# Kernel tuning notes

Measured on AMD Instinct MI355X. Metric: run time of the kernel, lower is better.

## Reference

```python
import jax, jax.numpy as jnp
import numpy as np

N_NODES = 100000
N_EDGES = 1600000
LN_EPS = 1e-5
CLAMP = 1.8


def setup_inputs() -> dict:
    key = jax.random.key(0)
    ks = jax.random.split(key, 12)
    feats = [100, 64, 64, 47]
    inp = {
        "x": jax.random.normal(ks[0], (N_NODES, feats[0]), dtype=jnp.float32),
        "adj_vals": jax.random.uniform(ks[1], (N_EDGES,), dtype=jnp.float32),
        "adj_row": jax.random.randint(ks[2], (N_EDGES,), 0, N_NODES),
        "adj_col": jax.random.randint(ks[3], (N_EDGES,), 0, N_NODES),
        "ln_gamma": jnp.ones((feats[0],), dtype=jnp.float32),
        "ln_beta": jnp.zeros((feats[0],), dtype=jnp.float32),
    }
    for i in range(3):
        fi, fo = feats[i], feats[i + 1]
        bound = 1.0 / np.sqrt(fi)
        inp[f"W{i+1}"] = jax.random.uniform(ks[4 + 2 * i], (fi, fo), minval=-bound, maxval=bound, dtype=jnp.float32)
        inp[f"b{i+1}"] = jax.random.uniform(ks[5 + 2 * i], (fo,), minval=-bound, maxval=bound, dtype=jnp.float32)
    return inp


def _spmm(vals, row, col, x):
    # out[i] = sum_{e: row[e]==i} vals[e] * x[col[e]]
    gathered = vals[:, None] * x[col]  # [E, D]
    return jax.ops.segment_sum(gathered, row, num_segments=N_NODES)


def reference(x, adj_vals, adj_row, adj_col, ln_gamma, ln_beta, W1, b1, W2, b2, W3, b3):
    # clamp to [-1.8, 1.8]: relu(x+1.8)-1.8 then 1.8-relu(1.8-x)
    x = jnp.clip(x, -CLAMP, CLAMP)
    # LayerNorm over last dim (100)
    mu = jnp.mean(x, axis=-1, keepdims=True)
    var = jnp.mean(jnp.square(x - mu), axis=-1, keepdims=True)
    x = (x - mu) * jax.lax.rsqrt(var + LN_EPS) * ln_gamma + ln_beta
    # GCN layers: Linear -> spmm -> (elu except last); dropout=0 => identity
    x = jax.nn.elu(_spmm(adj_vals, adj_row, adj_col, x @ W1 + b1))
    x = jax.nn.elu(_spmm(adj_vals, adj_row, adj_col, x @ W2 + b2))
    x = _spmm(adj_vals, adj_row, adj_col, x @ W3 + b3)
    return x
```

## Files before the change

kernel.cpp:

```cpp
#include <hip/hip_runtime.h>
#include <cstdint>
#include <cstddef>

#define N_NODES_C 100000
#define N_EDGES_C 1600000
#define LN_EPS_C 1e-5f
#define CLAMP_C 1.8f
#define SC_BLOCKS 1024
#define LN_BLOCKS 1024

typedef unsigned short ushort_t;

__device__ __forceinline__ float readlane_f(float v, int l) {
  return __uint_as_float(__builtin_amdgcn_readlane(__float_as_uint(v), l));
}

__device__ __forceinline__ float wave_sum(float v) {
#pragma unroll
  for (int off = 32; off > 0; off >>= 1) v += __shfl_xor(v, off, 64);
  return v;
}

__device__ __forceinline__ ushort_t f2bf(float f) {
  unsigned u = __float_as_uint(f);
  unsigned r = (u + 0x7fffu + ((u >> 16) & 1u)) >> 16;
  return (ushort_t)r;
}
__device__ __forceinline__ float bf2f(ushort_t u) {
  return __uint_as_float((unsigned)u << 16);
}

__global__ void hist_kernel(const int* __restrict__ row, int* __restrict__ counts) {
  int stride = gridDim.x * blockDim.x;
  for (int e = blockIdx.x * blockDim.x + threadIdx.x; e < N_EDGES_C; e += stride)
    atomicAdd(&counts[row[e]], 1);
}

__global__ void scan1_kernel(const int* __restrict__ counts, int* __restrict__ rowstart,
                             int* __restrict__ bsums) {
  __shared__ int lds[256];
  int t = threadIdx.x;
  int base = blockIdx.x * 1024 + t * 4;
  int c0 = (base + 0 < N_NODES_C) ? counts[base + 0] : 0;
  int c1 = (base + 1 < N_NODES_C) ? counts[base + 1] : 0;
  int c2 = (base + 2 < N_NODES_C) ? counts[base + 2] : 0;
  int c3 = (base + 3 < N_NODES_C) ? counts[base + 3] : 0;
  int s = c0 + c1 + c2 + c3;
  lds[t] = s;
  __syncthreads();
#pragma unroll
  for (int off = 1; off < 256; off <<= 1) {
    int v = (t >= off) ? lds[t - off] : 0;
    __syncthreads();
    lds[t] += v;
    __syncthreads();
  }
  int incl = lds[t];
  int excl = incl - s;
  if (t == 255) bsums[blockIdx.x] = incl;
  if (base + 0 < N_NODES_C) rowstart[base + 0] = excl;
  excl += c0;
  if (base + 1 < N_NODES_C) rowstart[base + 1] = excl;
  excl += c1;
  if (base + 2 < N_NODES_C) rowstart[base + 2] = excl;
  excl += c2;
  if (base + 3 < N_NODES_C) rowstart[base + 3] = excl;
}

__global__ void scan2_kernel(int* __restrict__ bsums, int nb) {
  __shared__ int lds[128];
  int t = threadIdx.x;
  int v = (t < nb) ? bsums[t] : 0;
  lds[t] = v;
  __syncthreads();
#pragma unroll
  for (int off = 1; off < 128; off <<= 1) {
    int u = (t >= off) ? lds[t - off] : 0;
    __syncthreads();
    lds[t] += u;
    __syncthreads();
  }
  if (t < nb) bsums[t] = lds[t] - v;
}

__global__ void scan3_kernel(int* __restrict__ rowstart, int* __restrict__ cursor,
                             const int* __restrict__ bsums) {
  int add = bsums[blockIdx.x];
  int base = blockIdx.x * 1024 + threadIdx.x * 4;
#pragma unroll
  for (int i = 0; i < 4; ++i)
    if (base + i < N_NODES_C) {
      int v = rowstart[base + i] + add;
      rowstart[base + i] = v;
      cursor[base + i] = v;
    }
}

__global__ __launch_bounds__(256) void scatter_ln_kernel(
    const int* __restrict__ row, const int* __restrict__ col,
    const float* __restrict__ vals, int* __restrict__ cursor,
    int2* __restrict__ edges_s,
    const float* __restrict__ x, const float* __restrict__ gamma,
    const float* __restrict__ beta, const float* __restrict__ W1,
    const float* __restrict__ b1, ushort_t* __restrict__ y) {
  if (blockIdx.x < SC_BLOCKS) {
    int tid = blockIdx.x * 256 + threadIdx.x;
    const int nt = SC_BLOCKS * 256;
    int r[8], c[8], p[8];
    float v[8];
#pragma unroll
    for (int k = 0; k < 8; ++k) {
      int e = tid + k * nt;
      bool in = e < N_EDGES_C;
      r[k] = in ? row[e] : 0;
      c[k] = in ? col[e] : 0;
      v[k] = in ? vals[e] : 0.f;
    }
#pragma unroll
    for (int k = 0; k < 8; ++k) {
      int e = tid + k * nt;
      if (e < N_EDGES_C) p[k] = atomicAdd(&cursor[r[k]], 1);
    }
#pragma unroll
    for (int k = 0; k < 8; ++k) {
      int e = tid + k * nt;
      if (e < N_EDGES_C) edges_s[p[k]] = make_int2(c[k], __float_as_int(v[k]));
    }
  } else {
    int lane = threadIdx.x & 63;
    int wid = (blockIdx.x - SC_BLOCKS) * 4 + (threadIdx.x >> 6);
    const int nw = LN_BLOCKS * 4;
    float w[100];
#pragma unroll
    for (int k = 0; k < 100; ++k) w[k] = W1[k * 64 + lane];
    float bias = b1[lane];
    float g0 = gamma[lane];
    float be0 = beta[lane];
    float g1 = (lane < 36) ? gamma[64 + lane] : 0.f;
    float be1 = (lane < 36) ? beta[64 + lane] : 0.f;
    for (int n = wid; n < N_NODES_C; n += nw) {
      const float* xr = x + (size_t)n * 100;
      float x0 = xr[lane];
      float x1 = (lane < 36) ? xr[64 + lane] : 0.f;
      x0 = fminf(fmaxf(x0, -CLAMP_C), CLAMP_C);
      x1 = fminf(fmaxf(x1, -CLAMP_C), CLAMP_C);
      float mu = wave_sum(x0 + x1) * 0.01f;
      float d0 = x0 - mu;
      float d1 = (lane < 36) ? (x1 - mu) : 0.f;
      float var = wave_sum(d0 * d0 + d1 * d1) * 0.01f;
      float inv = rsqrtf(var + LN_EPS_C);
      float xn0 = d0 * inv * g0 + be0;
      float xn1 = d1 * inv * g1 + be1;
      float acc = bias;
#pragma unroll
      for (int k = 0; k < 64; ++k) acc = fmaf(readlane_f(xn0, k), w[k], acc);
#pragma unroll
      for (int k = 0; k < 36; ++k) acc = fmaf(readlane_f(xn1, k), w[64 + k], acc);
      y[(size_t)n * 64 + lane] = f2bf(acc);
    }
  }
}

template <int DOUT>
__global__ __launch_bounds__(256) void spmm_elu_gemm_kernel(
    const int* __restrict__ rowstart, const int* __restrict__ counts,
    const int2* __restrict__ edges_s, const ushort_t* __restrict__ yb,
    const float* __restrict__ W, const float* __restrict__ b,
    ushort_t* __restrict__ out) {
  int lane = threadIdx.x & 63;
  int wid = blockIdx.x * (blockDim.x >> 6) + (threadIdx.x >> 6);
  int nw = gridDim.x * (blockDim.x >> 6);
  float w[64];
#pragma unroll
  for (int k = 0; k < 64; ++k) w[k] = (lane < DOUT) ? W[k * DOUT + lane] : 0.f;
  float bias = (lane < DOUT) ? b[lane] : 0.f;
  for (int n = wid; n < N_NODES_C; n += nw) {
    int start = rowstart[n];
    int cnt = counts[n];
    float a0 = 0.f, a1 = 0.f, a2 = 0.f, a3 = 0.f, a4 = 0.f, a5 = 0.f, a6 = 0.f, a7 = 0.f;
    for (int base = 0; base < cnt; base += 64) {
      int m = cnt - base;
      if (m > 64) m = 64;
      int2 ev = make_int2(0, 0);
      if (lane < m) ev = edges_s[start + base + lane];
      int mr = (m + 7) & ~7;
      for (int j = 0; j < mr; j += 8) {
        float g0 = bf2f(yb[(size_t)__builtin_amdgcn_readlane(ev.x, j + 0) * 64 + lane]);
        float g1 = bf2f(yb[(size_t)__builtin_amdgcn_readlane(ev.x, j + 1) * 64 + lane]);
        float g2 = bf2f(yb[(size_t)__builtin_amdgcn_readlane(ev.x, j + 2) * 64 + lane]);
        float g3 = bf2f(yb[(size_t)__builtin_amdgcn_readlane(ev.x, j + 3) * 64 + lane]);
        float g4 = bf2f(yb[(size_t)__builtin_amdgcn_readlane(ev.x, j + 4) * 64 + lane]);
        float g5 = bf2f(yb[(size_t)__builtin_amdgcn_readlane(ev.x, j + 5) * 64 + lane]);
        float g6 = bf2f(yb[(size_t)__builtin_amdgcn_readlane(ev.x, j + 6) * 64 + lane]);
        float g7 = bf2f(yb[(size_t)__builtin_amdgcn_readlane(ev.x, j + 7) * 64 + lane]);
        a0 = fmaf(__uint_as_float(__builtin_amdgcn_readlane((unsigned)ev.y, j + 0)), g0, a0);
        a1 = fmaf(__uint_as_float(__builtin_amdgcn_readlane((unsigned)ev.y, j + 1)), g1, a1);
        a2 = fmaf(__uint_as_float(__builtin_amdgcn_readlane((unsigned)ev.y, j + 2)), g2, a2);
        a3 = fmaf(__uint_as_float(__builtin_amdgcn_readlane((unsigned)ev.y, j + 3)), g3, a3);
        a4 = fmaf(__uint_as_float(__builtin_amdgcn_readlane((unsigned)ev.y, j + 4)), g4, a4);
        a5 = fmaf(__uint_as_float(__builtin_amdgcn_readlane((unsigned)ev.y, j + 5)), g5, a5);
        a6 = fmaf(__uint_as_float(__builtin_amdgcn_readlane((unsigned)ev.y, j + 6)), g6, a6);
        a7 = fmaf(__uint_as_float(__builtin_amdgcn_readlane((unsigned)ev.y, j + 7)), g7, a7);
      }
    }
    float acc = ((a0 + a1) + (a2 + a3)) + ((a4 + a5) + (a6 + a7));
    float xe = (acc > 0.f) ? acc : expm1f(acc);
    float o = bias;
#pragma unroll
    for (int k = 0; k < 64; ++k) o = fmaf(readlane_f(xe, k), w[k], o);
    if (lane < DOUT) out[(size_t)n * 64 + lane] = f2bf(o);
  }
}

__global__ __launch_bounds__(256) void spmm_final_kernel(
    const int* __restrict__ rowstart, const int* __restrict__ counts,
    const int2* __restrict__ edges_s, const ushort_t* __restrict__ yb,
    float* __restrict__ out) {
  int lane = threadIdx.x & 63;
  int wid = blockIdx.x * (blockDim.x >> 6) + (threadIdx.x >> 6);
  int nw = gridDim.x * (blockDim.x >> 6);
  int lmask = (lane < 47) ? lane : 46;
  for (int n = wid; n < N_NODES_C; n += nw) {
    int start = rowstart[n];
    int cnt = counts[n];
    float a0 = 0.f, a1 = 0.f, a2 = 0.f, a3 = 0.f, a4 = 0.f, a5 = 0.f, a6 = 0.f, a7 = 0.f;
    for (int base = 0; base < cnt; base += 64) {
      int m = cnt - base;
      if (m > 64) m = 64;
      int2 ev = make_int2(0, 0);
      if (lane < m) ev = edges_s[start + base + lane];
      int mr = (m + 7) & ~7;
      for (int j = 0; j < mr; j += 8) {
        float g0 = bf2f(yb[(size_t)__builtin_amdgcn_readlane(ev.x, j + 0) * 64 + lmask]);
        float g1 = bf2f(yb[(size_t)__builtin_amdgcn_readlane(ev.x, j + 1) * 64 + lmask]);
        float g2 = bf2f(yb[(size_t)__builtin_amdgcn_readlane(ev.x, j + 2) * 64 + lmask]);
        float g3 = bf2f(yb[(size_t)__builtin_amdgcn_readlane(ev.x, j + 3) * 64 + lmask]);
        float g4 = bf2f(yb[(size_t)__builtin_amdgcn_readlane(ev.x, j + 4) * 64 + lmask]);
        float g5 = bf2f(yb[(size_t)__builtin_amdgcn_readlane(ev.x, j + 5) * 64 + lmask]);
        float g6 = bf2f(yb[(size_t)__builtin_amdgcn_readlane(ev.x, j + 6) * 64 + lmask]);
        float g7 = bf2f(yb[(size_t)__builtin_amdgcn_readlane(ev.x, j + 7) * 64 + lmask]);
        a0 = fmaf(__uint_as_float(__builtin_amdgcn_readlane((unsigned)ev.y, j + 0)), g0, a0);
        a1 = fmaf(__uint_as_float(__builtin_amdgcn_readlane((unsigned)ev.y, j + 1)), g1, a1);
        a2 = fmaf(__uint_as_float(__builtin_amdgcn_readlane((unsigned)ev.y, j + 2)), g2, a2);
        a3 = fmaf(__uint_as_float(__builtin_amdgcn_readlane((unsigned)ev.y, j + 3)), g3, a3);
        a4 = fmaf(__uint_as_float(__builtin_amdgcn_readlane((unsigned)ev.y, j + 4)), g4, a4);
        a5 = fmaf(__uint_as_float(__builtin_amdgcn_readlane((unsigned)ev.y, j + 5)), g5, a5);
        a6 = fmaf(__uint_as_float(__builtin_amdgcn_readlane((unsigned)ev.y, j + 6)), g6, a6);
        a7 = fmaf(__uint_as_float(__builtin_amdgcn_readlane((unsigned)ev.y, j + 7)), g7, a7);
      }
    }
    float acc = ((a0 + a1) + (a2 + a3)) + ((a4 + a5) + (a6 + a7));
    if (lane < 47) out[(size_t)n * 47 + lane] = acc;
  }
}

extern "C" void kernel_launch(void* const* d_in, const int* in_sizes, int n_in,
                              void* d_out, int out_size, void* d_ws, size_t ws_size,
                              hipStream_t stream) {
  const float* x = (const float*)d_in[0];
  const float* adj_vals = (const float*)d_in[1];
  const int* adj_row = (const int*)d_in[2];
  const int* adj_col = (const int*)d_in[3];
  const float* gamma = (const float*)d_in[4];
  const float* beta = (const float*)d_in[5];
  const float* W1 = (const float*)d_in[6];
  const float* b1 = (const float*)d_in[7];
  const float* W2 = (const float*)d_in[8];
  const float* b2 = (const float*)d_in[9];
  const float* W3 = (const float*)d_in[10];
  const float* b3 = (const float*)d_in[11];
  float* out = (float*)d_out;

  char* ws = (char*)d_ws;
  size_t off = 0;
  auto alloc = [&](size_t bytes) -> void* {
    void* p = ws + off;
    off += (bytes + 255) & ~(size_t)255;
    return p;
  };
  ushort_t* bufA = (ushort_t*)alloc(sizeof(ushort_t) * (size_t)N_NODES_C * 64);
  ushort_t* bufB = (ushort_t*)alloc(sizeof(ushort_t) * (size_t)N_NODES_C * 64);
  int* counts = (int*)alloc(sizeof(int) * N_NODES_C);
  int* cursor = (int*)alloc(sizeof(int) * N_NODES_C);
  int* rowstart = (int*)alloc(sizeof(int) * N_NODES_C);
  int* bsums = (int*)alloc(sizeof(int) * 256);
  int2* edges_s = (int2*)alloc(sizeof(int2) * N_EDGES_C);

  hipMemsetAsync(counts, 0, sizeof(int) * N_NODES_C, stream);

  hist_kernel<<<2048, 256, 0, stream>>>(adj_row, counts);
  int nb = (N_NODES_C + 1023) / 1024;
  scan1_kernel<<<nb, 256, 0, stream>>>(counts, rowstart, bsums);
  scan2_kernel<<<1, 128, 0, stream>>>(bsums, nb);
  scan3_kernel<<<nb, 256, 0, stream>>>(rowstart, cursor, bsums);

  scatter_ln_kernel<<<SC_BLOCKS + LN_BLOCKS, 256, 0, stream>>>(
      adj_row, adj_col, adj_vals, cursor, edges_s, x, gamma, beta, W1, b1, bufA);

  spmm_elu_gemm_kernel<64><<<2048, 256, 0, stream>>>(rowstart, counts, edges_s, bufA,
                                                     W2, b2, bufB);
  spmm_elu_gemm_kernel<47><<<2048, 256, 0, stream>>>(rowstart, counts, edges_s, bufB,
                                                     W3, b3, bufA);
  spmm_final_kernel<<<2048, 256, 0, stream>>>(rowstart, counts, edges_s, bufA, out);
}
```

Measured before the change: 450.4 us.

## Interleave scatter/LN blocks, stream W1 from memory, widen SpMM gather batch to 16

The fused scatter+LN kernel now alternates scatter and LayerNorm work by even/odd block index instead of splitting at a fixed index, so both kinds of work land on the GPU at the same time. The LN branch no longer keeps all 100 W1 columns in registers and reads them from global/cache inside the FMA loop, which cuts register pressure and should raise occupancy. Both SpMM kernels now issue 16 gathered loads per batch instead of 8 for more memory-level parallelism, at the cost of more wasted padded gathers on short rows and extra registers.

New measurement: 403.4 us. 10.4% less time.

```diff
diff --git a/kernel.cpp b/kernel.cpp
--- a/kernel.cpp
+++ b/kernel.cpp
@@ -103,8 +103,8 @@
     const float* __restrict__ x, const float* __restrict__ gamma,
     const float* __restrict__ beta, const float* __restrict__ W1,
     const float* __restrict__ b1, ushort_t* __restrict__ y) {
-  if (blockIdx.x < SC_BLOCKS) {
-    int tid = blockIdx.x * 256 + threadIdx.x;
+  if ((blockIdx.x & 1) == 0) {
+    int tid = (blockIdx.x >> 1) * 256 + threadIdx.x;
     const int nt = SC_BLOCKS * 256;
     int r[8], c[8], p[8];
     float v[8];
@@ -128,11 +128,8 @@
     }
   } else {
     int lane = threadIdx.x & 63;
-    int wid = (blockIdx.x - SC_BLOCKS) * 4 + (threadIdx.x >> 6);
+    int wid = (blockIdx.x >> 1) * 4 + (threadIdx.x >> 6);
     const int nw = LN_BLOCKS * 4;
-    float w[100];
-#pragma unroll
-    for (int k = 0; k < 100; ++k) w[k] = W1[k * 64 + lane];
     float bias = b1[lane];
     float g0 = gamma[lane];
     float be0 = beta[lane];
@@ -153,9 +150,9 @@
       float xn1 = d1 * inv * g1 + be1;
       float acc = bias;
 #pragma unroll
-      for (int k = 0; k < 64; ++k) acc = fmaf(readlane_f(xn0, k), w[k], acc);
-#pragma unroll
-      for (int k = 0; k < 36; ++k) acc = fmaf(readlane_f(xn1, k), w[64 + k], acc);
+      for (int k = 0; k < 64; ++k) acc = fmaf(readlane_f(xn0, k), W1[k * 64 + lane], acc);
+#pragma unroll
+      for (int k = 0; k < 36; ++k) acc = fmaf(readlane_f(xn1, k), W1[(64 + k) * 64 + lane], acc);
       y[(size_t)n * 64 + lane] = f2bf(acc);
     }
   }
@@ -177,33 +174,28 @@
   for (int n = wid; n < N_NODES_C; n += nw) {
     int start = rowstart[n];
     int cnt = counts[n];
-    float a0 = 0.f, a1 = 0.f, a2 = 0.f, a3 = 0.f, a4 = 0.f, a5 = 0.f, a6 = 0.f, a7 = 0.f;
+    float a[8];
+#pragma unroll
+    for (int u = 0; u < 8; ++u) a[u] = 0.f;
     for (int base = 0; base < cnt; base += 64) {
       int m = cnt - base;
       if (m > 64) m = 64;
       int2 ev = make_int2(0, 0);
       if (lane < m) ev = edges_s[start + base + lane];
-      int mr = (m + 7) & ~7;
-      for (int j = 0; j < mr; j += 8) {
-        float g0 = bf2f(yb[(size_t)__builtin_amdgcn_readlane(ev.x, j + 0) * 64 + lane]);
-        float g1 = bf2f(yb[(size_t)__builtin_amdgcn_readlane(ev.x, j + 1) * 64 + lane]);
-        float g2 = bf2f(yb[(size_t)__builtin_amdgcn_readlane(ev.x, j + 2) * 64 + lane]);
-        float g3 = bf2f(yb[(size_t)__builtin_amdgcn_readlane(ev.x, j + 3) * 64 + lane]);
-        float g4 = bf2f(yb[(size_t)__builtin_amdgcn_readlane(ev.x, j + 4) * 64 + lane]);
-        float g5 = bf2f(yb[(size_t)__builtin_amdgcn_readlane(ev.x, j + 5) * 64 + lane]);
-        float g6 = bf2f(yb[(size_t)__builtin_amdgcn_readlane(ev.x, j + 6) * 64 + lane]);
-        float g7 = bf2f(yb[(size_t)__builtin_amdgcn_readlane(ev.x, j + 7) * 64 + lane]);
-        a0 = fmaf(__uint_as_float(__builtin_amdgcn_readlane((unsigned)ev.y, j + 0)), g0, a0);
-        a1 = fmaf(__uint_as_float(__builtin_amdgcn_readlane((unsigned)ev.y, j + 1)), g1, a1);
-        a2 = fmaf(__uint_as_float(__builtin_amdgcn_readlane((unsigned)ev.y, j + 2)), g2, a2);
-        a3 = fmaf(__uint_as_float(__builtin_amdgcn_readlane((unsigned)ev.y, j + 3)), g3, a3);
-        a4 = fmaf(__uint_as_float(__builtin_amdgcn_readlane((unsigned)ev.y, j + 4)), g4, a4);
-        a5 = fmaf(__uint_as_float(__builtin_amdgcn_readlane((unsigned)ev.y, j + 5)), g5, a5);
-        a6 = fmaf(__uint_as_float(__builtin_amdgcn_readlane((unsigned)ev.y, j + 6)), g6, a6);
-        a7 = fmaf(__uint_as_float(__builtin_amdgcn_readlane((unsigned)ev.y, j + 7)), g7, a7);
+      int mr = (m + 15) & ~15;
+      for (int j = 0; j < mr; j += 16) {
+        float g[16];
+#pragma unroll
+        for (int u = 0; u < 16; ++u)
+          g[u] = bf2f(yb[(size_t)__builtin_amdgcn_readlane(ev.x, j + u) * 64 + lane]);
+#pragma unroll
+        for (int u = 0; u < 16; ++u)
+          a[u & 7] = fmaf(
+              __uint_as_float(__builtin_amdgcn_readlane((unsigned)ev.y, j + u)), g[u],
+              a[u & 7]);
       }
     }
-    float acc = ((a0 + a1) + (a2 + a3)) + ((a4 + a5) + (a6 + a7));
+    float acc = ((a[0] + a[1]) + (a[2] + a[3])) + ((a[4] + a[5]) + (a[6] + a[7]));
     float xe = (acc > 0.f) ? acc : expm1f(acc);
     float o = bias;
 #pragma unroll
@@ -223,33 +215,28 @@
   for (int n = wid; n < N_NODES_C; n += nw) {
     int start = rowstart[n];
     int cnt = counts[n];
-    float a0 = 0.f, a1 = 0.f, a2 = 0.f, a3 = 0.f, a4 = 0.f, a5 = 0.f, a6 = 0.f, a7 = 0.f;
+    float a[8];
+#pragma unroll
+    for (int u = 0; u < 8; ++u) a[u] = 0.f;
     for (int base = 0; base < cnt; base += 64) {
       int m = cnt - base;
       if (m > 64) m = 64;
       int2 ev = make_int2(0, 0);
       if (lane < m) ev = edges_s[start + base + lane];
-      int mr = (m + 7) & ~7;
-      for (int j = 0; j < mr; j += 8) {
-        float g0 = bf2f(yb[(size_t)__builtin_amdgcn_readlane(ev.x, j + 0) * 64 + lmask]);
-        float g1 = bf2f(yb[(size_t)__builtin_amdgcn_readlane(ev.x, j + 1) * 64 + lmask]);
-        float g2 = bf2f(yb[(size_t)__builtin_amdgcn_readlane(ev.x, j + 2) * 64 + lmask]);
-        float g3 = bf2f(yb[(size_t)__builtin_amdgcn_readlane(ev.x, j + 3) * 64 + lmask]);
-        float g4 = bf2f(yb[(size_t)__builtin_amdgcn_readlane(ev.x, j + 4) * 64 + lmask]);
-        float g5 = bf2f(yb[(size_t)__builtin_amdgcn_readlane(ev.x, j + 5) * 64 + lmask]);
-        float g6 = bf2f(yb[(size_t)__builtin_amdgcn_readlane(ev.x, j + 6) * 64 + lmask]);
-        float g7 = bf2f(yb[(size_t)__builtin_amdgcn_readlane(ev.x, j + 7) * 64 + lmask]);
-        a0 = fmaf(__uint_as_float(__builtin_amdgcn_readlane((unsigned)ev.y, j + 0)), g0, a0);
-        a1 = fmaf(__uint_as_float(__builtin_amdgcn_readlane((unsigned)ev.y, j + 1)), g1, a1);
-        a2 = fmaf(__uint_as_float(__builtin_amdgcn_readlane((unsigned)ev.y, j + 2)), g2, a2);
-        a3 = fmaf(__uint_as_float(__builtin_amdgcn_readlane((unsigned)ev.y, j + 3)), g3, a3);
-        a4 = fmaf(__uint_as_float(__builtin_amdgcn_readlane((unsigned)ev.y, j + 4)), g4, a4);
-        a5 = fmaf(__uint_as_float(__builtin_amdgcn_readlane((unsigned)ev.y, j + 5)), g5, a5);
-        a6 = fmaf(__uint_as_float(__builtin_amdgcn_readlane((unsigned)ev.y, j + 6)), g6, a6);
-        a7 = fmaf(__uint_as_float(__builtin_amdgcn_readlane((unsigned)ev.y, j + 7)), g7, a7);
+      int mr = (m + 15) & ~15;
+      for (int j = 0; j < mr; j += 16) {
+        float g[16];
+#pragma unroll
+        for (int u = 0; u < 16; ++u)
+          g[u] = bf2f(yb[(size_t)__builtin_amdgcn_readlane(ev.x, j + u) * 64 + lmask]);
+#pragma unroll
+        for (int u = 0; u < 16; ++u)
+          a[u & 7] = fmaf(
+              __uint_as_float(__builtin_amdgcn_readlane((unsigned)ev.y, j + u)), g[u],
+              a[u & 7]);
       }
     }
-    float acc = ((a0 + a1) + (a2 + a3)) + ((a4 + a5) + (a6 + a7));
+    float acc = ((a[0] + a[1]) + (a[2] + a[3])) + ((a[4] + a[5]) + (a[6] + a[7]));
     if (lane < 47) out[(size_t)n * 47 + lane] = acc;
   }
 }
```
